# Performance work log

Hardware: AMD Instinct MI355X
Metric: run time of the kernel (lower is better)

## Reference

```python
import jax, jax.numpy as jnp
import numpy as np

D = 1024
DK = 1024
B, S = 4, 2048

def setup_inputs() -> dict:
    key = jax.random.key(0)
    ks = jax.random.split(key, 7)
    x = jax.random.normal(ks[0], (B, S, D), dtype=jnp.float32)
    mask = jnp.zeros((B, S, S), dtype=jnp.float32)
    scale = 1.0 / np.sqrt(D)
    Wq = jax.random.normal(ks[1], (D, DK), dtype=jnp.float32) * scale
    bq = jax.random.normal(ks[2], (DK,), dtype=jnp.float32) * 0.01
    Wk = jax.random.normal(ks[3], (D, DK), dtype=jnp.float32) * scale
    bk = jax.random.normal(ks[4], (DK,), dtype=jnp.float32) * 0.01
    Wv = jax.random.normal(ks[5], (D, DK), dtype=jnp.float32) * scale
    bv = jax.random.normal(ks[6], (DK,), dtype=jnp.float32) * 0.01
    return {"x": x, "mask": mask, "Wq": Wq, "bq": bq, "Wk": Wk, "bk": bk, "Wv": Wv, "bv": bv}

def reference(x, mask, Wq, bq, Wk, bk, Wv, bv):
    # Q/K/V projections: [B,S,D] @ [D,DK] + bias -> [B,S,DK]
    Q = jnp.einsum('bsd,dk->bsk', x, Wq) + bq
    K = jnp.einsum('bsd,dk->bsk', x, Wk) + bk
    V = jnp.einsum('bsd,dk->bsk', x, Wv) + bv
    scale = 1.0 / jnp.sqrt(jnp.asarray(DK, dtype=Q.dtype))
    scores = jnp.einsum('bqk,bpk->bqp', Q, K) * scale + mask  # [B,S,S]
    attn = jax.nn.softmax(scores, axis=-1)
    return jnp.einsum('bqp,bpk->bqk', attn, V)
```

## Files before the change

kernel.cpp:

```cpp
#include <hip/hip_runtime.h>
#include <hip/hip_bf16.h>
#include <stdint.h>

typedef unsigned short u16;
typedef __attribute__((ext_vector_type(4))) unsigned short u16x4;
typedef __attribute__((ext_vector_type(8))) short short8;
typedef __attribute__((ext_vector_type(4))) float f32x4;

__device__ inline u16 f2b(float f) {
  uint32_t u = __builtin_bit_cast(uint32_t, f);
  u += 0x7fffu + ((u >> 16) & 1u);
  return (u16)(u >> 16);
}
__device__ inline float b2f(u16 b) {
  return __builtin_bit_cast(float, (uint32_t)b << 16);
}

__global__ __launch_bounds__(256) void prep(
    const float* __restrict__ x, u16* __restrict__ xb,
    const float* __restrict__ Wq, const float* __restrict__ Wk,
    const float* __restrict__ Wv, u16* __restrict__ wT,
    const float* __restrict__ bq, const float* __restrict__ bk,
    const float* __restrict__ bv, float* __restrict__ biasC,
    float* __restrict__ rowsum) {
  __shared__ float tl[32][33];
  const int b = blockIdx.x;
  const int t = threadIdx.x;
  if (b < 8192) {
    long i = ((long)b * 256 + t) * 4;
    float4 v = *(const float4*)(x + i);
    u16x4 o = { f2b(v.x), f2b(v.y), f2b(v.z), f2b(v.w) };
    *(u16x4*)(xb + i) = o;
  } else if (b < 8192 + 3072) {
    const int bb = b - 8192;
    const int z = bb >> 10;
    const int tile = bb & 1023;
    const float* in = z == 0 ? Wq : (z == 1 ? Wk : Wv);
    u16* o = wT + (long)z * 1024 * 1024;
    const int c0 = (tile & 31) * 32, r0 = (tile >> 5) * 32;
    const int tx = t & 31, ty = t >> 5;
#pragma unroll
    for (int j = 0; j < 32; j += 8)
      tl[ty + j][tx] = in[(long)(r0 + ty + j) * 1024 + c0 + tx];
    __syncthreads();
#pragma unroll
    for (int j = 0; j < 32; j += 8)
      o[(long)(c0 + ty + j) * 1024 + r0 + tx] = f2b(tl[tx][ty + j]);
  } else {
    const int i = (b - 8192 - 3072) * 256 + t;
    if (i < 3072)
      biasC[i] = i < 1024 ? bq[i] : (i < 2048 ? bk[i - 1024] : bv[i - 2048]);
    else if (i < 3072 + 8192)
      rowsum[i - 3072] = 0.0f;
  }
}

__device__ inline void load_lds16(const void* g, void* l) {
  __builtin_amdgcn_global_load_lds((const __attribute__((address_space(1))) void*)g,
                                   (__attribute__((address_space(3))) void*)l, 16, 0, 0);
}

#define BAR  asm volatile("s_barrier" ::: "memory")
#define LGK0 asm volatile("s_waitcnt lgkmcnt(0)" ::: "memory")
#define VM4  asm volatile("s_waitcnt vmcnt(4)" ::: "memory")

#define MM(IH, JH) do {                                                        \
  __builtin_amdgcn_s_setprio(1);                                               \
  _Pragma("unroll")                                                            \
  for (int i_ = 0; i_ < 4; i_++)                                               \
    _Pragma("unroll")                                                          \
    for (int j_ = 0; j_ < 2; j_++)                                             \
      _Pragma("unroll")                                                        \
      for (int kk_ = 0; kk_ < 2; kk_++)                                        \
        acc[(IH)*4 + i_][(JH)*2 + j_] = __builtin_amdgcn_mfma_f32_16x16x32_bf16( \
            aF[i_][kk_], bF[j_][kk_], acc[(IH)*4 + i_][(JH)*2 + j_], 0, 0, 0); \
  __builtin_amdgcn_s_setprio(0);                                               \
} while (0)

template <int MODE>
__global__ __launch_bounds__(512, 1) void gemm8(
    const u16* __restrict__ A, const u16* __restrict__ Bt, void* __restrict__ C,
    u16* __restrict__ vtOut, const float* __restrict__ bias,
    float* __restrict__ rsum, const float* __restrict__ maskG,
    int K, int lda, int ldb, int ldc,
    long sA_, long sB_, long sC_, float scale)
{
  const int z = blockIdx.z;
  A += z * sA_;
  Bt += z * sB_;
  const long cbase = z * sC_;

  __shared__ __align__(16) u16 sA[2][256 * 64];
  __shared__ __align__(16) u16 sB[2][256 * 64];

  const int t = threadIdx.x;
  const int lane = t & 63, wave = t >> 6;
  const int wr = wave >> 2, wc = wave & 3;
  const int fr = lane & 15, q4 = lane >> 4;
  const int m0 = blockIdx.y * 256, n0 = blockIdx.x * 256;
  const int nT = K / 64;

  auto stA = [&](int half, int kt, int buf) {
    if (kt >= nT) kt = 0;
    const long ko = (long)kt * 64;
#pragma unroll
    for (int ii = 0; ii < 2; ii++) {
      int c = ii * 512 + t;
      int rr = c >> 3, slot = c & 7;
      int row = (rr < 64) ? (half * 64 + rr) : (128 + half * 64 + rr - 64);
      int gch = slot ^ (row & 7);
      load_lds16(A + (long)(m0 + row) * lda + ko + gch * 8,
                 &sA[buf][row * 64 + slot * 8]);
    }
  };
  auto stB = [&](int half, int kt, int buf) {
    if (kt >= nT) kt = 0;
    const long ko = (long)kt * 64;
#pragma unroll
    for (int ii = 0; ii < 2; ii++) {
      int c = ii * 512 + t;
      int rr = c >> 3, slot = c & 7;
      int row = (rr >> 5) * 64 + half * 32 + (rr & 31);
      int gch = slot ^ (row & 7);
      load_lds16(Bt + (long)(n0 + row) * ldb + ko + gch * 8,
                 &sB[buf][row * 64 + slot * 8]);
    }
  };

  short8 aF[4][2], bF[2][2];
  f32x4 acc[8][4] = {};

  auto rdA = [&](int half, int buf) {
#pragma unroll
    for (int i = 0; i < 4; i++) {
      int row = wr * 128 + half * 64 + i * 16 + fr;
#pragma unroll
      for (int kk = 0; kk < 2; kk++) {
        int ch = kk * 4 + q4;
        aF[i][kk] = *(const short8*)&sA[buf][row * 64 + ((ch ^ (row & 7)) * 8)];
      }
    }
  };
  auto rdB = [&](int half, int buf) {
#pragma unroll
    for (int j = 0; j < 2; j++) {
      int row = wc * 64 + half * 32 + j * 16 + fr;
#pragma unroll
      for (int kk = 0; kk < 2; kk++) {
        int ch = kk * 4 + q4;
        bF[j][kk] = *(const short8*)&sB[buf][row * 64 + ((ch ^ (row & 7)) * 8)];
      }
    }
  };

  stA(0, 0, 0); stB(0, 0, 0); stB(1, 0, 0); stA(1, 0, 0);
  VM4; BAR;

  const int nIt = nT / 2;
#pragma unroll 1
  for (int it = 0; it < nIt; ++it) {
    const int kt = 2 * it;
    rdA(0, 0); rdB(0, 0); stA(0, kt + 1, 1);
    BAR; LGK0; MM(0, 0); VM4; BAR;
    rdB(1, 0);            stB(0, kt + 1, 1);
    BAR; LGK0; MM(0, 1); VM4; BAR;
    rdA(1, 0);            stB(1, kt + 1, 1);
    BAR; LGK0; MM(1, 1);      BAR;
    rdB(0, 0);            stA(1, kt + 1, 1);
    BAR; LGK0; MM(1, 0); VM4; BAR;
    rdA(0, 1); rdB(0, 1); stA(0, kt + 2, 0);
    BAR; LGK0; MM(0, 0); VM4; BAR;
    rdB(1, 1);            stB(0, kt + 2, 0);
    BAR; LGK0; MM(0, 1); VM4; BAR;
    rdA(1, 1);            stB(1, kt + 2, 0);
    BAR; LGK0; MM(1, 1);      BAR;
    rdB(0, 1);            stA(1, kt + 2, 0);
    BAR; LGK0; MM(1, 0); VM4; BAR;
  }

  if (MODE == 2) {
    const float* mk = maskG + (long)z * 2048 * 2048;
    u16* Pout = (u16*)C + cbase;
    float* rz = rsum + (long)z * 2048;
#pragma unroll
    for (int i = 0; i < 8; i++) {
      const int row = m0 + wr * 128 + i * 16 + q4 * 4;
      float ml[4][4];
#pragma unroll
      for (int j = 0; j < 4; j++) {
        const int col = n0 + wc * 64 + j * 16 + fr;
#pragma unroll
        for (int r = 0; r < 4; r++)
          ml[j][r] = mk[(long)(row + r) * 2048 + col];
      }
      float rs[4] = {0.f, 0.f, 0.f, 0.f};
#pragma unroll
      for (int j = 0; j < 4; j++) {
        const int col = n0 + wc * 64 + j * 16 + fr;
#pragma unroll
        for (int r = 0; r < 4; r++) {
          float e = __expf(acc[i][j][r] * scale + ml[j][r]);
          Pout[(long)(row + r) * ldc + col] = f2b(e);
          rs[r] += e;
        }
      }
#pragma unroll
      for (int r = 0; r < 4; r++) {
        float s = rs[r];
        s += __shfl_xor(s, 1); s += __shfl_xor(s, 2);
        s += __shfl_xor(s, 4); s += __shfl_xor(s, 8);
        if (fr == 0) atomicAdd(&rz[row + r], s);
      }
    }
  } else {
#pragma unroll
    for (int i = 0; i < 8; i++) {
#pragma unroll
      for (int j = 0; j < 4; j++) {
        const int row = m0 + wr * 128 + i * 16 + q4 * 4;
        const int col = n0 + wc * 64 + j * 16 + fr;
        const float b = bias[col];
        if (col >= 2048) {
          u16x4 o = { f2b(acc[i][j][0] + b), f2b(acc[i][j][1] + b),
                      f2b(acc[i][j][2] + b), f2b(acc[i][j][3] + b) };
          *(u16x4*)(vtOut + (long)(col - 2048) * 8192 + row) = o;
        } else {
#pragma unroll
          for (int r = 0; r < 4; r++)
            ((u16*)C)[(long)(row + r) * ldc + col] = f2b(acc[i][j][r] + b);
        }
      }
    }
  }
}

#define BM 128
#define BN 128
#define BK 64

__global__ __launch_bounds__(256, 2) void gemm_pv(
    const u16* __restrict__ A, const u16* __restrict__ Bt, float* __restrict__ C,
    const float* __restrict__ rsum,
    int K, int lda, int ldb, int ldc, long sA_, long sB_, long sC_)
{
  const int z = blockIdx.z;
  A += z * sA_;
  Bt += z * sB_;
  const long cbase = z * sC_;

  __shared__ __align__(16) u16 lA[BM * BK];
  __shared__ __align__(16) u16 lB[BN * BK];

  const int t = threadIdx.x;
  const int lane = t & 63;
  const int wave = t >> 6;
  const int wr = wave >> 1, wc = wave & 1;
  const int m0 = blockIdx.y * BM, n0 = blockIdx.x * BN;

  const int srow = t >> 3;
  const int schunk = (t & 7) ^ (srow & 7);
  const u16* aS = A + (long)(m0 + srow) * lda + schunk * 8;
  const u16* bS = Bt + (long)(n0 + srow) * ldb + schunk * 8;

  f32x4 acc[4][4] = {};
  const int fr = lane & 15;
  const int q4 = lane >> 4;

  for (int k0 = 0; k0 < K; k0 += BK) {
    __syncthreads();
#pragma unroll
    for (int i = 0; i < 4; i++) {
      load_lds16(aS + k0 + (long)(i * 32) * lda, &lA[(i * 256 + t) * 8]);
      load_lds16(bS + k0 + (long)(i * 32) * ldb, &lB[(i * 256 + t) * 8]);
    }
    __syncthreads();
#pragma unroll
    for (int kk = 0; kk < 2; kk++) {
      const int ch = kk * 4 + q4;
      short8 aF[4], bF[4];
#pragma unroll
      for (int i = 0; i < 4; i++) {
        int row = wr * 64 + i * 16 + fr;
        aF[i] = *(const short8*)&lA[row * BK + ((ch ^ (row & 7)) * 8)];
      }
#pragma unroll
      for (int j = 0; j < 4; j++) {
        int row = wc * 64 + j * 16 + fr;
        bF[j] = *(const short8*)&lB[row * BK + ((ch ^ (row & 7)) * 8)];
      }
#pragma unroll
      for (int i = 0; i < 4; i++)
#pragma unroll
        for (int j = 0; j < 4; j++)
          acc[i][j] = __builtin_amdgcn_mfma_f32_16x16x32_bf16(aF[i], bF[j], acc[i][j], 0, 0, 0);
    }
  }

  const int r0 = q4 * 4;
  const float* lz = rsum + (long)z * 2048;
#pragma unroll
  for (int i = 0; i < 4; i++) {
    const int row = m0 + wr * 64 + i * 16 + r0;
    float inv[4];
#pragma unroll
    for (int r = 0; r < 4; r++) inv[r] = 1.0f / lz[row + r];
#pragma unroll
    for (int j = 0; j < 4; j++) {
      const int col = n0 + wc * 64 + j * 16 + fr;
#pragma unroll
      for (int r = 0; r < 4; r++)
        C[cbase + (long)(row + r) * ldc + col] = acc[i][j][r] * inv[r];
    }
  }
}

extern "C" void kernel_launch(void* const* d_in, const int* in_sizes, int n_in,
                              void* d_out, int out_size, void* d_ws, size_t ws_size,
                              hipStream_t stream) {
  const float* x    = (const float*)d_in[0];
  const float* mask = (const float*)d_in[1];
  const float* Wq   = (const float*)d_in[2];
  const float* bq   = (const float*)d_in[3];
  const float* Wk   = (const float*)d_in[4];
  const float* bk   = (const float*)d_in[5];
  const float* Wv   = (const float*)d_in[6];
  const float* bv   = (const float*)d_in[7];
  float* out = (float*)d_out;

  char* w = (char*)d_ws;
  u16*   xb    = (u16*)(w);
  u16*   wT    = (u16*)(w + 16777216);
  float* biasC = (float*)(w + 23068672);
  u16*   QKV   = (u16*)(w + 23081088);
  u16*   Vt    = (u16*)(w + 73414016);
  u16*   Pp    = (u16*)(w + 90191232);
  float* rowsum= (float*)(w + 123745664);

  prep<<<8192 + 3072 + 44, 256, 0, stream>>>(x, xb, Wq, Wk, Wv, wT, bq, bk, bv, biasC, rowsum);

  gemm8<0><<<dim3(12, 32, 1), 512, 0, stream>>>(xb, wT, QKV, Vt, biasC, nullptr, nullptr,
      1024, 1024, 1024, 3072, 0, 0, 0, 1.0f);

  gemm8<2><<<dim3(8, 8, 4), 512, 0, stream>>>(QKV, QKV + 1024, Pp, nullptr, nullptr, rowsum,
      mask,
      1024, 3072, 3072, 2048,
      2048L * 3072, 2048L * 3072, 2048L * 2048, 0.03125f);

  gemm_pv<<<dim3(8, 16, 4), 256, 0, stream>>>(Pp, Vt, out, rowsum,
      2048, 2048, 8192, 1024,
      2048L * 2048, 2048L, 2048L * 1024);
}
```

Baseline: 313.2 us.

## Split QKV projection into a 128x128 GEMM and re-pipeline the scores GEMM

The QKV projection moves from the 256x256 eight-wave gemm8 kernel to a simpler 128x128 four-wave kernel with two blocks per CU. The grid grows from 384 to 1536 blocks, which is meant to give better CU occupancy and wave balance on the 8192x3072 output. The scores kernel gets a new software pipeline with one k-tile per iteration. It prefetches two tiles ahead, keeps B fragments for both halves in registers, and removes the explicit lgkmcnt waits. The loss of those waits risks LDS read ordering issues, and the deeper prefetch adds register pressure.

```diff
diff --git a/kernel.cpp b/kernel.cpp
--- a/kernel.cpp
+++ b/kernel.cpp
@@ -61,10 +61,88 @@
 }
 
 #define BAR  asm volatile("s_barrier" ::: "memory")
-#define LGK0 asm volatile("s_waitcnt lgkmcnt(0)" ::: "memory")
 #define VM4  asm volatile("s_waitcnt vmcnt(4)" ::: "memory")
-
-#define MM(IH, JH) do {                                                        \
+#define VM6  asm volatile("s_waitcnt vmcnt(6)" ::: "memory")
+
+#define BM 128
+#define BN 128
+#define BK 64
+
+__global__ __launch_bounds__(256, 2) void gemm_qkv(
+    const u16* __restrict__ A, const u16* __restrict__ Bt, u16* __restrict__ C,
+    u16* __restrict__ vtOut, const float* __restrict__ bias,
+    int K, int lda, int ldb, int ldc)
+{
+  __shared__ __align__(16) u16 lA[BM * BK];
+  __shared__ __align__(16) u16 lB[BN * BK];
+
+  const int t = threadIdx.x;
+  const int lane = t & 63;
+  const int wave = t >> 6;
+  const int wr = wave >> 1, wc = wave & 1;
+  const int m0 = blockIdx.y * BM, n0 = blockIdx.x * BN;
+
+  const int srow = t >> 3;
+  const int schunk = (t & 7) ^ (srow & 7);
+  const u16* aS = A + (long)(m0 + srow) * lda + schunk * 8;
+  const u16* bS = Bt + (long)(n0 + srow) * ldb + schunk * 8;
+
+  f32x4 acc[4][4] = {};
+  const int fr = lane & 15;
+  const int q4 = lane >> 4;
+
+  for (int k0 = 0; k0 < K; k0 += BK) {
+    __syncthreads();
+#pragma unroll
+    for (int i = 0; i < 4; i++) {
+      load_lds16(aS + k0 + (long)(i * 32) * lda, &lA[(i * 256 + t) * 8]);
+      load_lds16(bS + k0 + (long)(i * 32) * ldb, &lB[(i * 256 + t) * 8]);
+    }
+    __syncthreads();
+#pragma unroll
+    for (int kk = 0; kk < 2; kk++) {
+      const int ch = kk * 4 + q4;
+      short8 aF[4], bF[4];
+#pragma unroll
+      for (int i = 0; i < 4; i++) {
+        int row = wr * 64 + i * 16 + fr;
+        aF[i] = *(const short8*)&lA[row * BK + ((ch ^ (row & 7)) * 8)];
+      }
+#pragma unroll
+      for (int j = 0; j < 4; j++) {
+        int row = wc * 64 + j * 16 + fr;
+        bF[j] = *(const short8*)&lB[row * BK + ((ch ^ (row & 7)) * 8)];
+      }
+#pragma unroll
+      for (int i = 0; i < 4; i++)
+#pragma unroll
+        for (int j = 0; j < 4; j++)
+          acc[i][j] = __builtin_amdgcn_mfma_f32_16x16x32_bf16(aF[i], bF[j], acc[i][j], 0, 0, 0);
+    }
+  }
+
+  const int r0 = q4 * 4;
+#pragma unroll
+  for (int i = 0; i < 4; i++) {
+#pragma unroll
+    for (int j = 0; j < 4; j++) {
+      const int row = m0 + wr * 64 + i * 16 + r0;
+      const int col = n0 + wc * 64 + j * 16 + fr;
+      const float b = bias[col];
+      if (col >= 2048) {
+        u16x4 o = { f2b(acc[i][j][0] + b), f2b(acc[i][j][1] + b),
+                    f2b(acc[i][j][2] + b), f2b(acc[i][j][3] + b) };
+        *(u16x4*)(vtOut + (long)(col - 2048) * 8192 + row) = o;
+      } else {
+#pragma unroll
+        for (int r = 0; r < 4; r++)
+          C[(long)(row + r) * ldc + col] = f2b(acc[i][j][r] + b);
+      }
+    }
+  }
+}
+
+#define MM8(IH, JH) do {                                                       \
   __builtin_amdgcn_s_setprio(1);                                               \
   _Pragma("unroll")                                                            \
   for (int i_ = 0; i_ < 4; i_++)                                               \
@@ -73,14 +151,12 @@
       _Pragma("unroll")                                                        \
       for (int kk_ = 0; kk_ < 2; kk_++)                                        \
         acc[(IH)*4 + i_][(JH)*2 + j_] = __builtin_amdgcn_mfma_f32_16x16x32_bf16( \
-            aF[i_][kk_], bF[j_][kk_], acc[(IH)*4 + i_][(JH)*2 + j_], 0, 0, 0); \
+            aF[i_][kk_], bF[JH][j_][kk_], acc[(IH)*4 + i_][(JH)*2 + j_], 0, 0, 0); \
   __builtin_amdgcn_s_setprio(0);                                               \
 } while (0)
 
-template <int MODE>
-__global__ __launch_bounds__(512, 1) void gemm8(
-    const u16* __restrict__ A, const u16* __restrict__ Bt, void* __restrict__ C,
-    u16* __restrict__ vtOut, const float* __restrict__ bias,
+__global__ __launch_bounds__(512, 1) void gemm8s(
+    const u16* __restrict__ A, const u16* __restrict__ Bt, u16* __restrict__ P,
     float* __restrict__ rsum, const float* __restrict__ maskG,
     int K, int lda, int ldb, int ldc,
     long sA_, long sB_, long sC_, float scale)
@@ -101,7 +177,7 @@
   const int nT = K / 64;
 
   auto stA = [&](int half, int kt, int buf) {
-    if (kt >= nT) kt = 0;
+    if (kt >= nT) kt -= nT;
     const long ko = (long)kt * 64;
 #pragma unroll
     for (int ii = 0; ii < 2; ii++) {
@@ -114,7 +190,7 @@
     }
   };
   auto stB = [&](int half, int kt, int buf) {
-    if (kt >= nT) kt = 0;
+    if (kt >= nT) kt -= nT;
     const long ko = (long)kt * 64;
 #pragma unroll
     for (int ii = 0; ii < 2; ii++) {
@@ -127,7 +203,8 @@
     }
   };
 
-  short8 aF[4][2], bF[2][2];
+  short8 aF[4][2];
+  short8 bF[2][2][2];
   f32x4 acc[8][4] = {};
 
   auto rdA = [&](int half, int buf) {
@@ -148,95 +225,63 @@
 #pragma unroll
       for (int kk = 0; kk < 2; kk++) {
         int ch = kk * 4 + q4;
-        bF[j][kk] = *(const short8*)&sB[buf][row * 64 + ((ch ^ (row & 7)) * 8)];
+        bF[half][j][kk] = *(const short8*)&sB[buf][row * 64 + ((ch ^ (row & 7)) * 8)];
       }
     }
   };
 
   stA(0, 0, 0); stB(0, 0, 0); stB(1, 0, 0); stA(1, 0, 0);
-  VM4; BAR;
-
-  const int nIt = nT / 2;
+  VM4;
+  stA(0, 1, 1); stB(0, 1, 1); stB(1, 1, 1);
+  VM6; BAR;
+
 #pragma unroll 1
-  for (int it = 0; it < nIt; ++it) {
-    const int kt = 2 * it;
-    rdA(0, 0); rdB(0, 0); stA(0, kt + 1, 1);
-    BAR; LGK0; MM(0, 0); VM4; BAR;
-    rdB(1, 0);            stB(0, kt + 1, 1);
-    BAR; LGK0; MM(0, 1); VM4; BAR;
-    rdA(1, 0);            stB(1, kt + 1, 1);
-    BAR; LGK0; MM(1, 1);      BAR;
-    rdB(0, 0);            stA(1, kt + 1, 1);
-    BAR; LGK0; MM(1, 0); VM4; BAR;
-    rdA(0, 1); rdB(0, 1); stA(0, kt + 2, 0);
-    BAR; LGK0; MM(0, 0); VM4; BAR;
-    rdB(1, 1);            stB(0, kt + 2, 0);
-    BAR; LGK0; MM(0, 1); VM4; BAR;
-    rdA(1, 1);            stB(1, kt + 2, 0);
-    BAR; LGK0; MM(1, 1);      BAR;
-    rdB(0, 1);            stA(1, kt + 2, 0);
-    BAR; LGK0; MM(1, 0); VM4; BAR;
-  }
-
-  if (MODE == 2) {
-    const float* mk = maskG + (long)z * 2048 * 2048;
-    u16* Pout = (u16*)C + cbase;
-    float* rz = rsum + (long)z * 2048;
-#pragma unroll
-    for (int i = 0; i < 8; i++) {
-      const int row = m0 + wr * 128 + i * 16 + q4 * 4;
-      float ml[4][4];
-#pragma unroll
-      for (int j = 0; j < 4; j++) {
-        const int col = n0 + wc * 64 + j * 16 + fr;
-#pragma unroll
-        for (int r = 0; r < 4; r++)
-          ml[j][r] = mk[(long)(row + r) * 2048 + col];
-      }
-      float rs[4] = {0.f, 0.f, 0.f, 0.f};
-#pragma unroll
-      for (int j = 0; j < 4; j++) {
-        const int col = n0 + wc * 64 + j * 16 + fr;
-#pragma unroll
-        for (int r = 0; r < 4; r++) {
-          float e = __expf(acc[i][j][r] * scale + ml[j][r]);
-          Pout[(long)(row + r) * ldc + col] = f2b(e);
-          rs[r] += e;
-        }
-      }
+  for (int kt = 0; kt < nT; ++kt) {
+    const int buf = kt & 1, nbuf = buf ^ 1;
+    rdA(0, buf); rdB(0, buf); stA(1, kt + 1, nbuf);
+    BAR; MM8(0, 0); BAR;
+    rdB(1, buf);              stA(0, kt + 2, buf);
+    BAR; MM8(0, 1); BAR;
+    rdA(1, buf);              stB(0, kt + 2, buf);
+    BAR; MM8(1, 1); BAR;
+    stB(1, kt + 2, buf);
+    BAR; MM8(1, 0); VM6; BAR;
+  }
+
+  const float* mk = maskG + (long)z * 2048 * 2048;
+  u16* Pout = P + cbase;
+  float* rz = rsum + (long)z * 2048;
+#pragma unroll
+  for (int i = 0; i < 8; i++) {
+    const int row = m0 + wr * 128 + i * 16 + q4 * 4;
+    float ml[4][4];
+#pragma unroll
+    for (int j = 0; j < 4; j++) {
+      const int col = n0 + wc * 64 + j * 16 + fr;
+#pragma unroll
+      for (int r = 0; r < 4; r++)
+        ml[j][r] = mk[(long)(row + r) * 2048 + col];
+    }
+    float rs[4] = {0.f, 0.f, 0.f, 0.f};
+#pragma unroll
+    for (int j = 0; j < 4; j++) {
+      const int col = n0 + wc * 64 + j * 16 + fr;
 #pragma unroll
       for (int r = 0; r < 4; r++) {
-        float s = rs[r];
-        s += __shfl_xor(s, 1); s += __shfl_xor(s, 2);
-        s += __shfl_xor(s, 4); s += __shfl_xor(s, 8);
-        if (fr == 0) atomicAdd(&rz[row + r], s);
-      }
-    }
-  } else {
-#pragma unroll
-    for (int i = 0; i < 8; i++) {
-#pragma unroll
-      for (int j = 0; j < 4; j++) {
-        const int row = m0 + wr * 128 + i * 16 + q4 * 4;
-        const int col = n0 + wc * 64 + j * 16 + fr;
-        const float b = bias[col];
-        if (col >= 2048) {
-          u16x4 o = { f2b(acc[i][j][0] + b), f2b(acc[i][j][1] + b),
-                      f2b(acc[i][j][2] + b), f2b(acc[i][j][3] + b) };
-          *(u16x4*)(vtOut + (long)(col - 2048) * 8192 + row) = o;
-        } else {
-#pragma unroll
-          for (int r = 0; r < 4; r++)
-            ((u16*)C)[(long)(row + r) * ldc + col] = f2b(acc[i][j][r] + b);
-        }
-      }
-    }
-  }
-}
-
-#define BM 128
-#define BN 128
-#define BK 64
+        float e = __expf(acc[i][j][r] * scale + ml[j][r]);
+        Pout[(long)(row + r) * ldc + col] = f2b(e);
+        rs[r] += e;
+      }
+    }
+#pragma unroll
+    for (int r = 0; r < 4; r++) {
+      float s = rs[r];
+      s += __shfl_xor(s, 1); s += __shfl_xor(s, 2);
+      s += __shfl_xor(s, 4); s += __shfl_xor(s, 8);
+      if (fr == 0) atomicAdd(&rz[row + r], s);
+    }
+  }
+}
 
 __global__ __launch_bounds__(256, 2) void gemm_pv(
     const u16* __restrict__ A, const u16* __restrict__ Bt, float* __restrict__ C,
@@ -338,11 +383,10 @@
 
   prep<<<8192 + 3072 + 44, 256, 0, stream>>>(x, xb, Wq, Wk, Wv, wT, bq, bk, bv, biasC, rowsum);
 
-  gemm8<0><<<dim3(12, 32, 1), 512, 0, stream>>>(xb, wT, QKV, Vt, biasC, nullptr, nullptr,
-      1024, 1024, 1024, 3072, 0, 0, 0, 1.0f);
-
-  gemm8<2><<<dim3(8, 8, 4), 512, 0, stream>>>(QKV, QKV + 1024, Pp, nullptr, nullptr, rowsum,
-      mask,
+  gemm_qkv<<<dim3(24, 64, 1), 256, 0, stream>>>(xb, wT, QKV, Vt, biasC,
+      1024, 1024, 1024, 3072);
+
+  gemm8s<<<dim3(8, 8, 4), 512, 0, stream>>>(QKV, QKV + 1024, Pp, rowsum, mask,
       1024, 3072, 3072, 2048,
       2048L * 3072, 2048L * 3072, 2048L * 2048, 0.03125f);
 
```

New measurement: 302.8 us. 3.3% less time.

## Deepen gemm8 prefetch pipeline and remap blocks XCD-aware across all GEMMs

Applied to the files above, without the earlier changes.

Restructures the gemm8 main loop from a two-k-tile unrolled body with explicit lgkmcnt waits into a one-k-tile loop. That loop prefetches tiles up to two k-steps ahead, holds both B fragment halves in registers, and uses a deeper vmcnt(6) wait. All three GEMM launches also switch to a 1-D grid that is remapped so consecutive blocks on the same XCD (b&7) cover neighbouring tiles, which should improve L2 locality. The goal is more overlap between global loads and MFMA and fewer cross-XCD cache misses. In exchange it uses more registers, and dropping the explicit LDS waits relies on the barriers and compiler-inserted waits to keep ordering correct.

```diff
diff --git a/kernel.cpp b/kernel.cpp
--- a/kernel.cpp
+++ b/kernel.cpp
@@ -11,9 +11,6 @@
   uint32_t u = __builtin_bit_cast(uint32_t, f);
   u += 0x7fffu + ((u >> 16) & 1u);
   return (u16)(u >> 16);
-}
-__device__ inline float b2f(u16 b) {
-  return __builtin_bit_cast(float, (uint32_t)b << 16);
 }
 
 __global__ __launch_bounds__(256) void prep(
@@ -61,10 +58,10 @@
 }
 
 #define BAR  asm volatile("s_barrier" ::: "memory")
-#define LGK0 asm volatile("s_waitcnt lgkmcnt(0)" ::: "memory")
 #define VM4  asm volatile("s_waitcnt vmcnt(4)" ::: "memory")
-
-#define MM(IH, JH) do {                                                        \
+#define VM6  asm volatile("s_waitcnt vmcnt(6)" ::: "memory")
+
+#define MM8(IH, JH) do {                                                       \
   __builtin_amdgcn_s_setprio(1);                                               \
   _Pragma("unroll")                                                            \
   for (int i_ = 0; i_ < 4; i_++)                                               \
@@ -73,7 +70,7 @@
       _Pragma("unroll")                                                        \
       for (int kk_ = 0; kk_ < 2; kk_++)                                        \
         acc[(IH)*4 + i_][(JH)*2 + j_] = __builtin_amdgcn_mfma_f32_16x16x32_bf16( \
-            aF[i_][kk_], bF[j_][kk_], acc[(IH)*4 + i_][(JH)*2 + j_], 0, 0, 0); \
+            aF[i_][kk_], bF[JH][j_][kk_], acc[(IH)*4 + i_][(JH)*2 + j_], 0, 0, 0); \
   __builtin_amdgcn_s_setprio(0);                                               \
 } while (0)
 
@@ -83,9 +80,14 @@
     u16* __restrict__ vtOut, const float* __restrict__ bias,
     float* __restrict__ rsum, const float* __restrict__ maskG,
     int K, int lda, int ldb, int ldc,
-    long sA_, long sB_, long sC_, float scale)
+    long sA_, long sB_, long sC_, float scale,
+    int swq, int tpz, int nx)
 {
-  const int z = blockIdx.z;
+  const int b = blockIdx.x;
+  const int s = (b & 7) * swq + (b >> 3);
+  const int z = s / tpz, rem = s % tpz;
+  const int bx = rem % nx, by = rem / nx;
+
   A += z * sA_;
   Bt += z * sB_;
   const long cbase = z * sC_;
@@ -97,11 +99,11 @@
   const int lane = t & 63, wave = t >> 6;
   const int wr = wave >> 2, wc = wave & 3;
   const int fr = lane & 15, q4 = lane >> 4;
-  const int m0 = blockIdx.y * 256, n0 = blockIdx.x * 256;
+  const int m0 = by * 256, n0 = bx * 256;
   const int nT = K / 64;
 
   auto stA = [&](int half, int kt, int buf) {
-    if (kt >= nT) kt = 0;
+    if (kt >= nT) kt -= nT;
     const long ko = (long)kt * 64;
 #pragma unroll
     for (int ii = 0; ii < 2; ii++) {
@@ -114,7 +116,7 @@
     }
   };
   auto stB = [&](int half, int kt, int buf) {
-    if (kt >= nT) kt = 0;
+    if (kt >= nT) kt -= nT;
     const long ko = (long)kt * 64;
 #pragma unroll
     for (int ii = 0; ii < 2; ii++) {
@@ -127,7 +129,8 @@
     }
   };
 
-  short8 aF[4][2], bF[2][2];
+  short8 aF[4][2];
+  short8 bF[2][2][2];
   f32x4 acc[8][4] = {};
 
   auto rdA = [&](int half, int buf) {
@@ -148,34 +151,27 @@
 #pragma unroll
       for (int kk = 0; kk < 2; kk++) {
         int ch = kk * 4 + q4;
-        bF[j][kk] = *(const short8*)&sB[buf][row * 64 + ((ch ^ (row & 7)) * 8)];
+        bF[half][j][kk] = *(const short8*)&sB[buf][row * 64 + ((ch ^ (row & 7)) * 8)];
       }
     }
   };
 
   stA(0, 0, 0); stB(0, 0, 0); stB(1, 0, 0); stA(1, 0, 0);
-  VM4; BAR;
-
-  const int nIt = nT / 2;
+  VM4;
+  stA(0, 1, 1); stB(0, 1, 1); stB(1, 1, 1);
+  VM6; BAR;
+
 #pragma unroll 1
-  for (int it = 0; it < nIt; ++it) {
-    const int kt = 2 * it;
-    rdA(0, 0); rdB(0, 0); stA(0, kt + 1, 1);
-    BAR; LGK0; MM(0, 0); VM4; BAR;
-    rdB(1, 0);            stB(0, kt + 1, 1);
-    BAR; LGK0; MM(0, 1); VM4; BAR;
-    rdA(1, 0);            stB(1, kt + 1, 1);
-    BAR; LGK0; MM(1, 1);      BAR;
-    rdB(0, 0);            stA(1, kt + 1, 1);
-    BAR; LGK0; MM(1, 0); VM4; BAR;
-    rdA(0, 1); rdB(0, 1); stA(0, kt + 2, 0);
-    BAR; LGK0; MM(0, 0); VM4; BAR;
-    rdB(1, 1);            stB(0, kt + 2, 0);
-    BAR; LGK0; MM(0, 1); VM4; BAR;
-    rdA(1, 1);            stB(1, kt + 2, 0);
-    BAR; LGK0; MM(1, 1);      BAR;
-    rdB(0, 1);            stA(1, kt + 2, 0);
-    BAR; LGK0; MM(1, 0); VM4; BAR;
+  for (int kt = 0; kt < nT; ++kt) {
+    const int buf = kt & 1, nbuf = buf ^ 1;
+    rdA(0, buf); rdB(0, buf); stA(1, kt + 1, nbuf);
+    BAR; MM8(0, 0); BAR;
+    rdB(1, buf);              stA(0, kt + 2, buf);
+    BAR; MM8(0, 1); BAR;
+    rdA(1, buf);              stB(0, kt + 2, buf);
+    BAR; MM8(1, 1); BAR;
+    stB(1, kt + 2, buf);
+    BAR; MM8(1, 0); VM6; BAR;
   }
 
   if (MODE == 2) {
@@ -206,10 +202,10 @@
       }
 #pragma unroll
       for (int r = 0; r < 4; r++) {
-        float s = rs[r];
-        s += __shfl_xor(s, 1); s += __shfl_xor(s, 2);
-        s += __shfl_xor(s, 4); s += __shfl_xor(s, 8);
-        if (fr == 0) atomicAdd(&rz[row + r], s);
+        float s2 = rs[r];
+        s2 += __shfl_xor(s2, 1); s2 += __shfl_xor(s2, 2);
+        s2 += __shfl_xor(s2, 4); s2 += __shfl_xor(s2, 8);
+        if (fr == 0) atomicAdd(&rz[row + r], s2);
       }
     }
   } else {
@@ -219,15 +215,15 @@
       for (int j = 0; j < 4; j++) {
         const int row = m0 + wr * 128 + i * 16 + q4 * 4;
         const int col = n0 + wc * 64 + j * 16 + fr;
-        const float b = bias[col];
+        const float b2 = bias[col];
         if (col >= 2048) {
-          u16x4 o = { f2b(acc[i][j][0] + b), f2b(acc[i][j][1] + b),
-                      f2b(acc[i][j][2] + b), f2b(acc[i][j][3] + b) };
+          u16x4 o = { f2b(acc[i][j][0] + b2), f2b(acc[i][j][1] + b2),
+                      f2b(acc[i][j][2] + b2), f2b(acc[i][j][3] + b2) };
           *(u16x4*)(vtOut + (long)(col - 2048) * 8192 + row) = o;
         } else {
 #pragma unroll
           for (int r = 0; r < 4; r++)
-            ((u16*)C)[(long)(row + r) * ldc + col] = f2b(acc[i][j][r] + b);
+            ((u16*)C)[(long)(row + r) * ldc + col] = f2b(acc[i][j][r] + b2);
         }
       }
     }
@@ -241,9 +237,14 @@
 __global__ __launch_bounds__(256, 2) void gemm_pv(
     const u16* __restrict__ A, const u16* __restrict__ Bt, float* __restrict__ C,
     const float* __restrict__ rsum,
-    int K, int lda, int ldb, int ldc, long sA_, long sB_, long sC_)
+    int K, int lda, int ldb, int ldc, long sA_, long sB_, long sC_,
+    int swq, int tpz, int nx)
 {
-  const int z = blockIdx.z;
+  const int b = blockIdx.x;
+  const int s = (b & 7) * swq + (b >> 3);
+  const int z = s / tpz, rem = s % tpz;
+  const int bx = rem % nx, by = rem / nx;
+
   A += z * sA_;
   Bt += z * sB_;
   const long cbase = z * sC_;
@@ -255,7 +256,7 @@
   const int lane = t & 63;
   const int wave = t >> 6;
   const int wr = wave >> 1, wc = wave & 1;
-  const int m0 = blockIdx.y * BM, n0 = blockIdx.x * BN;
+  const int m0 = by * BM, n0 = bx * BN;
 
   const int srow = t >> 3;
   const int schunk = (t & 7) ^ (srow & 7);
@@ -338,15 +339,17 @@
 
   prep<<<8192 + 3072 + 44, 256, 0, stream>>>(x, xb, Wq, Wk, Wv, wT, bq, bk, bv, biasC, rowsum);
 
-  gemm8<0><<<dim3(12, 32, 1), 512, 0, stream>>>(xb, wT, QKV, Vt, biasC, nullptr, nullptr,
-      1024, 1024, 1024, 3072, 0, 0, 0, 1.0f);
-
-  gemm8<2><<<dim3(8, 8, 4), 512, 0, stream>>>(QKV, QKV + 1024, Pp, nullptr, nullptr, rowsum,
-      mask,
+  gemm8<0><<<384, 512, 0, stream>>>(xb, wT, QKV, Vt, biasC, nullptr, nullptr,
+      1024, 1024, 1024, 3072, 0, 0, 0, 1.0f,
+      48, 384, 12);
+
+  gemm8<2><<<256, 512, 0, stream>>>(QKV, QKV + 1024, Pp, nullptr, nullptr, rowsum, mask,
       1024, 3072, 3072, 2048,
-      2048L * 3072, 2048L * 3072, 2048L * 2048, 0.03125f);
-
-  gemm_pv<<<dim3(8, 16, 4), 256, 0, stream>>>(Pp, Vt, out, rowsum,
+      2048L * 3072, 2048L * 3072, 2048L * 2048, 0.03125f,
+      32, 64, 8);
+
+  gemm_pv<<<512, 256, 0, stream>>>(Pp, Vt, out, rowsum,
       2048, 2048, 8192, 1024,
-      2048L * 2048, 2048L, 2048L * 1024);
-}
+      2048L * 2048, 2048L, 2048L * 1024,
+      64, 128, 8);
+}
```

Result: faster. 306.6 us (-2.1%).
